# Kernel tuning notes

Hardware: AMD Instinct MI355X
Metric: run time of the kernel (lower is better)

The kernel has to match this reference:

```python
import jax, jax.numpy as jnp
import numpy as np

B, N, IN_C, OUT_C = 32, 1024, 64, 128
ALPHA = 0.2  # LeakyReLU negative slope
NEG_INF = -1e16


def setup_inputs() -> dict:
    key = jax.random.key(0)
    k1, k2, k3, k4, k5 = jax.random.split(key, 5)
    inputs = jax.random.normal(k1, (B, N, IN_C), dtype=jnp.float32)
    # dense 0/1 adjacency mask
    graph = jax.random.randint(k2, (N, N), 0, 2).astype(jnp.float32)
    # torch nn.Linear weight layout: [out_c, in_c]
    W = jax.random.normal(k3, (OUT_C, IN_C), dtype=jnp.float32)
    b = jax.random.normal(k4, (OUT_C,), dtype=jnp.float32)
    a = jax.random.normal(k5, (2 * OUT_C, 1), dtype=jnp.float32)
    return {"inputs": inputs, "graph": graph, "W": W, "b": b, "a": a}


def reference(inputs, graph, W, b, a):
    # h = W(inputs): [B, N, D]
    h = jnp.einsum('bnt,dt->bnd', inputs, W)
    # cat([h_i, h_j]) @ a  ==  h_i @ a1 + h_j @ a2  (decomposed, no [B,N,N,2D] tensor)
    a1 = a[:OUT_C, 0]   # [D]
    a2 = a[OUT_C:, 0]   # [D]
    s1 = jnp.einsum('bnd,d->bn', h, a1)  # score contribution of node i
    s2 = jnp.einsum('bnd,d->bn', h, a2)  # score contribution of node j
    e = s1[:, :, None] + s2[:, None, :]  # [B, N, N]
    e = jnp.where(e > 0, e, ALPHA * e)   # LeakyReLU
    e = e * graph                        # zero out non-edges
    # torch masked_fill_(eq(outputs, 0), -1e16)
    e = jnp.where(e == 0.0, NEG_INF, e)
    attention = jax.nn.softmax(e, axis=2)  # [B, N, N]
    out = jnp.einsum('bij,bjd->bid', attention, h) + b  # [B, N, D]
    return out
```

## Files before the change

kernel.cpp:

```cpp
#include <hip/hip_runtime.h>
#include <hip/hip_bf16.h>

#define ALPHA 0.2f

typedef unsigned short ushort_t;
typedef unsigned int   uint_t;
typedef unsigned short ushort8 __attribute__((ext_vector_type(8)));
typedef uint_t uintv4 __attribute__((ext_vector_type(4)));
typedef float f32x4 __attribute__((ext_vector_type(4)));
typedef __bf16 bf16x8 __attribute__((ext_vector_type(8)));

__device__ __forceinline__ ushort_t f2bf(float f) {
  unsigned u = __float_as_uint(f);
  u += 0x7fffu + ((u >> 16) & 1u);
  return (ushort_t)(u >> 16);
}

__global__ __launch_bounds__(256) void gat_pack_kernel(
    const float* __restrict__ graph, const float* __restrict__ W,
    const float* __restrict__ avec, uint_t* __restrict__ gmask,
    float* __restrict__ u)
{
  const int row = blockIdx.x, t = threadIdx.x;
  __shared__ uint_t nibs[256];
  float4 g = ((const float4*)(graph + (size_t)row * 1024))[t];
  uint_t nib = (g.x != 0.f ? 1u : 0u) | (g.y != 0.f ? 2u : 0u) |
               (g.z != 0.f ? 4u : 0u) | (g.w != 0.f ? 8u : 0u);
  nibs[t] = nib;
  __syncthreads();
  if (t < 32) {
    uint_t wd = 0;
#pragma unroll
    for (int k = 0; k < 8; ++k) wd |= nibs[t * 8 + k] << (4 * k);
    gmask[(size_t)row * 32 + t] = wd;
  }
  if (row == 0 && t < 128) {
    const int k  = t & 63;
    const int ao = (t >> 6) * 128;
    float a0 = 0.f, a1 = 0.f, a2 = 0.f, a3 = 0.f;
    for (int d = 0; d < 128; d += 4) {
      a0 = fmaf(avec[ao + d + 0], W[(d + 0) * 64 + k], a0);
      a1 = fmaf(avec[ao + d + 1], W[(d + 1) * 64 + k], a1);
      a2 = fmaf(avec[ao + d + 2], W[(d + 2) * 64 + k], a2);
      a3 = fmaf(avec[ao + d + 3], W[(d + 3) * 64 + k], a3);
    }
    u[t] = (a0 + a1) + (a2 + a3);
  }
}

__global__ __launch_bounds__(256) void gat_h_kernel(
    const float* __restrict__ inp, const float* __restrict__ W,
    const float* __restrict__ uvec, ushort_t* __restrict__ hT,
    float* __restrict__ s1, float* __restrict__ s2)
{
  const int b  = blockIdx.x >> 5;
  const int n0 = (blockIdx.x & 31) << 5;
  const int t  = threadIdx.x;
  const int d  = t & 127;
  const int nh = t >> 7;

  __shared__ float    x_lds[32][68];
  __shared__ float    u_lds[128];
  __shared__ ushort_t h_tile[128][40];

  float wreg[64];
  {
    const float4* wrow = (const float4*)(W + d * 64);
#pragma unroll
    for (int k = 0; k < 16; ++k) {
      float4 v = wrow[k];
      wreg[4*k+0] = v.x; wreg[4*k+1] = v.y; wreg[4*k+2] = v.z; wreg[4*k+3] = v.w;
    }
  }
  if (t < 128) u_lds[t] = uvec[t];

  {
    const float4* xsrc = (const float4*)(inp + ((size_t)b * 1024 + n0) * 64);
#pragma unroll
    for (int k = 0; k < 2; ++k) {
      const int g = k * 256 + t;
      const int n = g >> 4, c = g & 15;
      *(float4*)&x_lds[n][c * 4] = xsrc[g];
    }
  }
  __syncthreads();

  for (int r = 0; r < 16; ++r) {
    const int n = nh * 16 + r;
    const float* xr = &x_lds[n][0];
    float ax = 0.f, ay = 0.f, az = 0.f, aw = 0.f;
#pragma unroll
    for (int k = 0; k < 16; ++k) {
      float4 xv = *(const float4*)&xr[4 * k];
      ax = fmaf(wreg[4*k+0], xv.x, ax);
      ay = fmaf(wreg[4*k+1], xv.y, ay);
      az = fmaf(wreg[4*k+2], xv.z, az);
      aw = fmaf(wreg[4*k+3], xv.w, aw);
    }
    h_tile[d][n] = f2bf((ax + ay) + (az + aw));
  }

  if (t < 64) {
    const int n = t & 31, which = t >> 5;
    const float* xr = &x_lds[n][0];
    const float* uu = &u_lds[which * 64];
    float a0 = 0.f, a1 = 0.f, a2 = 0.f, a3 = 0.f;
#pragma unroll
    for (int k = 0; k < 16; ++k) {
      float4 xv = *(const float4*)&xr[4 * k];
      a0 = fmaf(xv.x, uu[4*k+0], a0);
      a1 = fmaf(xv.y, uu[4*k+1], a1);
      a2 = fmaf(xv.z, uu[4*k+2], a2);
      a3 = fmaf(xv.w, uu[4*k+3], a3);
    }
    const float sv = (a0 + a1) + (a2 + a3);
    if (which == 0) s1[(size_t)b * 1024 + n0 + n] = sv;
    else            s2[(size_t)b * 1024 + n0 + n] = sv;
  }
  __syncthreads();

#pragma unroll
  for (int it = 0; it < 2; ++it) {
    const int idx = it * 256 + t;
    const int d2  = idx >> 2;
    const int ch  = (idx & 3) * 8;
    ushort8 v = *(const ushort8*)&h_tile[d2][ch];
    *(ushort8*)(hT + ((size_t)b * 128 + d2) * 1024 + n0 + ch) = v;
  }
}

__global__ __launch_bounds__(256) void gat_attn_kernel(
    const uint_t* __restrict__ gmask, const ushort_t* __restrict__ hT,
    const float* __restrict__ s1g, const float* __restrict__ s2g,
    const float* __restrict__ bias, float* __restrict__ out)
{
  const int ic = blockIdx.x;
  const int b  = blockIdx.y;
  const int i0 = ic << 6;
  const int t  = threadIdx.x;
  const int w  = t >> 6;
  const int rg = w & 1;
  const int jh = w >> 1;
  const int l  = t & 63;
  const int rl = l & 15;
  const int js = (l >> 4) * 8;

  __shared__ float  s2_lds[1024];
  __shared__ uint_t mask_lds[64][33];
  __shared__ float  red_part[64][4];
  __shared__ float  red_row[64];
  __shared__ float  credu[64][132];
  __shared__ float  den_lds[64];

  ((float4*)s2_lds)[t] = ((const float4*)(s2g + (size_t)b * 1024))[t];
  {
    const uint4* gsrc = (const uint4*)(gmask + (size_t)i0 * 32);
#pragma unroll
    for (int k2 = 0; k2 < 2; ++k2) {
      const int idx = t + k2 * 256;
      uint4 mv = gsrc[idx];
      const int mr = idx >> 3, mc = (idx & 7) * 4;
      mask_lds[mr][mc + 0] = mv.x; mask_lds[mr][mc + 1] = mv.y;
      mask_lds[mr][mc + 2] = mv.z; mask_lds[mr][mc + 3] = mv.w;
    }
  }
  __syncthreads();

  {
    const int irow = t >> 2, bo = (t & 3) * 8;
    float mx = -1e30f;
    for (int jt = 0; jt < 32; ++jt) {
      const uint_t wd = mask_lds[irow][jt] >> bo;
      const float4 sA = *(const float4*)(s2_lds + jt * 32 + bo);
      const float4 sB = *(const float4*)(s2_lds + jt * 32 + bo + 4);
      if (wd & 1u)   mx = fmaxf(mx, sA.x);
      if (wd & 2u)   mx = fmaxf(mx, sA.y);
      if (wd & 4u)   mx = fmaxf(mx, sA.z);
      if (wd & 8u)   mx = fmaxf(mx, sA.w);
      if (wd & 16u)  mx = fmaxf(mx, sB.x);
      if (wd & 32u)  mx = fmaxf(mx, sB.y);
      if (wd & 64u)  mx = fmaxf(mx, sB.z);
      if (wd & 128u) mx = fmaxf(mx, sB.w);
    }
    red_part[irow][t & 3] = mx;
  }
  __syncthreads();
  if (t < 64)
    red_row[t] = fmaxf(fmaxf(red_part[t][0], red_part[t][1]),
                       fmaxf(red_part[t][2], red_part[t][3]));
  __syncthreads();

  const int ib = rg * 32;
  const float s1lo = s1g[(size_t)b * 1024 + i0 + ib + rl];
  const float s1hi = s1g[(size_t)b * 1024 + i0 + ib + 16 + rl];
  const float tl = s1lo + red_row[ib + rl];
  const float th = s1hi + red_row[ib + 16 + rl];
  const float Milo = tl > 0.f ? tl : ALPHA * tl;
  const float Mihi = th > 0.f ? th : ALPHA * th;

  const ushort_t* hb =
      hT + (size_t)b * 128 * 1024 + (size_t)rl * 1024 + jh * 512 + js;

  f32x4 c[2][8];
#pragma unroll
  for (int is = 0; is < 2; ++is)
#pragma unroll
    for (int ds = 0; ds < 8; ++ds) c[is][ds] = f32x4{0.f, 0.f, 0.f, 0.f};
  float den_lo = 0.f, den_hi = 0.f;

  ushort8 bv[8], nb[8];
#pragma unroll
  for (int ds = 0; ds < 8; ++ds)
    bv[ds] = *(const ushort8*)(hb + (size_t)ds * 16 * 1024);

  for (int jt = 0; jt < 16; ++jt) {
    const int j0 = jt * 32;
    const int jn = (jt + 1 < 16) ? j0 + 32 : j0;
#pragma unroll
    for (int ds = 0; ds < 8; ++ds)
      nb[ds] = *(const ushort8*)(hb + (size_t)ds * 16 * 1024 + jn);

    const uint_t wlo = mask_lds[ib + rl][jh * 16 + jt] >> js;
    const uint_t whi = mask_lds[ib + 16 + rl][jh * 16 + jt] >> js;
    const float4 sA = *(const float4*)(s2_lds + jh * 512 + j0 + js);
    const float4 sB = *(const float4*)(s2_lds + jh * 512 + j0 + js + 4);
    const float sv[8] = {sA.x, sA.y, sA.z, sA.w, sB.x, sB.y, sB.z, sB.w};
    float plo[8], phi[8];
#pragma unroll
    for (int e = 0; e < 8; ++e) {
      float te = s1lo + sv[e];
      float v  = fmaxf(te, ALPHA * te);
      plo[e] = (((wlo >> e) & 1u) && v != 0.f) ? __expf(v - Milo) : 0.f;
      te = s1hi + sv[e];
      v  = fmaxf(te, ALPHA * te);
      phi[e] = (((whi >> e) & 1u) && v != 0.f) ? __expf(v - Mihi) : 0.f;
    }
    uint_t pkl[4], pkh[4];
#pragma unroll
    for (int q = 0; q < 4; ++q) {
      asm("v_cvt_pk_bf16_f32 %0, %1, %2"
          : "=v"(pkl[q]) : "v"(plo[2 * q]), "v"(plo[2 * q + 1]));
      asm("v_cvt_pk_bf16_f32 %0, %1, %2"
          : "=v"(pkh[q]) : "v"(phi[2 * q]), "v"(phi[2 * q + 1]));
      den_lo += __uint_as_float(pkl[q] << 16) +
                __uint_as_float(pkl[q] & 0xffff0000u);
      den_hi += __uint_as_float(pkh[q] << 16) +
                __uint_as_float(pkh[q] & 0xffff0000u);
    }
    const bf16x8 av0 =
        __builtin_bit_cast(bf16x8, (uintv4){pkl[0], pkl[1], pkl[2], pkl[3]});
    const bf16x8 av1 =
        __builtin_bit_cast(bf16x8, (uintv4){pkh[0], pkh[1], pkh[2], pkh[3]});
    __builtin_amdgcn_s_setprio(1);
#pragma unroll
    for (int ds = 0; ds < 8; ++ds) {
      const bf16x8 bvv = __builtin_bit_cast(bf16x8, bv[ds]);
      c[0][ds] = __builtin_amdgcn_mfma_f32_16x16x32_bf16(av0, bvv, c[0][ds], 0, 0, 0);
      c[1][ds] = __builtin_amdgcn_mfma_f32_16x16x32_bf16(av1, bvv, c[1][ds], 0, 0, 0);
    }
    __builtin_amdgcn_s_setprio(0);
#pragma unroll
    for (int ds = 0; ds < 8; ++ds) bv[ds] = nb[ds];
  }

  den_lo += __shfl_xor(den_lo, 16); den_lo += __shfl_xor(den_lo, 32);
  den_hi += __shfl_xor(den_hi, 16); den_hi += __shfl_xor(den_hi, 32);

  if (jh == 1) {
#pragma unroll
    for (int is = 0; is < 2; ++is)
#pragma unroll
      for (int ds = 0; ds < 8; ++ds)
#pragma unroll
        for (int r = 0; r < 4; ++r)
          credu[ib + is * 16 + (l >> 4) * 4 + r][ds * 16 + rl] = c[is][ds][r];
    if (l < 16) {
      den_lds[ib + rl]      = den_lo;
      den_lds[ib + 16 + rl] = den_hi;
    }
  }
  __syncthreads();
  if (jh == 0) {
    const float dl = den_lo + den_lds[ib + rl];
    const float dh = den_hi + den_lds[ib + 16 + rl];
    const float inv_lo = dl > 0.f ? 1.f / dl : 0.f;
    const float inv_hi = dh > 0.f ? 1.f / dh : 0.f;
#pragma unroll
    for (int ds = 0; ds < 8; ++ds) {
      const int col = ds * 16 + rl;
      const float bc = bias[col];
#pragma unroll
      for (int is = 0; is < 2; ++is) {
#pragma unroll
        for (int r = 0; r < 4; ++r) {
          const int rr  = (l >> 4) * 4 + r;
          const int row = ib + is * 16 + rr;
          const float cc = c[is][ds][r] + credu[row][col];
          const float iv = __shfl(is ? inv_hi : inv_lo, rr);
          out[((size_t)b * 1024 + i0 + row) * 128 + col] = fmaf(cc, iv, bc);
        }
      }
    }
  }
}

extern "C" void kernel_launch(void* const* d_in, const int* in_sizes, int n_in,
                              void* d_out, int out_size, void* d_ws, size_t ws_size,
                              hipStream_t stream) {
  (void)in_sizes; (void)n_in; (void)out_size; (void)ws_size;
  const float* inp   = (const float*)d_in[0];
  const float* graph = (const float*)d_in[1];
  const float* W     = (const float*)d_in[2];
  const float* bias  = (const float*)d_in[3];
  const float* avec  = (const float*)d_in[4];
  float* out = (float*)d_out;

  char* ws = (char*)d_ws;
  ushort_t* hT = (ushort_t*)ws;
  float* s1    = (float*)(ws + (size_t)8 * 1024 * 1024);
  float* s2    = s1 + 32 * 1024;
  float* u     = s2 + 32 * 1024;
  uint_t* gm   = (uint_t*)(ws + (size_t)8 * 1024 * 1024 + 512 * 1024);

  gat_pack_kernel<<<1024, 256, 0, stream>>>(graph, W, avec, gm, u);
  gat_h_kernel<<<1024, 256, 0, stream>>>(inp, W, u, hT, s1, s2);
  gat_attn_kernel<<<dim3(16, 32), 256, 0, stream>>>(gm, hT, s1, s2, bias, out);
}
```

Baseline: 75.40 us.

## Compute softmax denominator via MFMA with ones, prefetch mask/s2 and split max chains

The softmax denominator is now accumulated by two extra MFMAs against a vector of bf16 ones, replacing the scalar bf16 unpack-and-add and the cross-lane shuffles. The per-tile mask words and s2 values are loaded from LDS one iteration ahead, overlapping LDS latency with compute. The row-max loop keeps four independent accumulators to break the serial fmax dependency chain. This adds 2 MFMAs per tile (about 12% more matrix work) and extra registers for the prefetched values, in exchange for fewer VALU ops and shorter dependency chains.

Result: no change. 74.51 us (-1.2%).

```diff
diff --git a/kernel.cpp b/kernel.cpp
--- a/kernel.cpp
+++ b/kernel.cpp
@@ -168,21 +168,27 @@
 
   {
     const int irow = t >> 2, bo = (t & 3) * 8;
-    float mx = -1e30f;
-    for (int jt = 0; jt < 32; ++jt) {
-      const uint_t wd = mask_lds[irow][jt] >> bo;
-      const float4 sA = *(const float4*)(s2_lds + jt * 32 + bo);
-      const float4 sB = *(const float4*)(s2_lds + jt * 32 + bo + 4);
-      if (wd & 1u)   mx = fmaxf(mx, sA.x);
-      if (wd & 2u)   mx = fmaxf(mx, sA.y);
-      if (wd & 4u)   mx = fmaxf(mx, sA.z);
-      if (wd & 8u)   mx = fmaxf(mx, sA.w);
-      if (wd & 16u)  mx = fmaxf(mx, sB.x);
-      if (wd & 32u)  mx = fmaxf(mx, sB.y);
-      if (wd & 64u)  mx = fmaxf(mx, sB.z);
-      if (wd & 128u) mx = fmaxf(mx, sB.w);
-    }
-    red_part[irow][t & 3] = mx;
+    float mxa[4] = {-1e30f, -1e30f, -1e30f, -1e30f};
+    for (int jt4 = 0; jt4 < 8; ++jt4) {
+#pragma unroll
+      for (int q = 0; q < 4; ++q) {
+        const int jt = jt4 * 4 + q;
+        const uint_t wd = mask_lds[irow][jt] >> bo;
+        const float4 sA = *(const float4*)(s2_lds + jt * 32 + bo);
+        const float4 sB = *(const float4*)(s2_lds + jt * 32 + bo + 4);
+        float m = mxa[q];
+        if (wd & 1u)   m = fmaxf(m, sA.x);
+        if (wd & 2u)   m = fmaxf(m, sA.y);
+        if (wd & 4u)   m = fmaxf(m, sA.z);
+        if (wd & 8u)   m = fmaxf(m, sA.w);
+        if (wd & 16u)  m = fmaxf(m, sB.x);
+        if (wd & 32u)  m = fmaxf(m, sB.y);
+        if (wd & 64u)  m = fmaxf(m, sB.z);
+        if (wd & 128u) m = fmaxf(m, sB.w);
+        mxa[q] = m;
+      }
+    }
+    red_part[irow][t & 3] = fmaxf(fmaxf(mxa[0], mxa[1]), fmaxf(mxa[2], mxa[3]));
   }
   __syncthreads();
   if (t < 64)
@@ -206,12 +212,19 @@
   for (int is = 0; is < 2; ++is)
 #pragma unroll
     for (int ds = 0; ds < 8; ++ds) c[is][ds] = f32x4{0.f, 0.f, 0.f, 0.f};
-  float den_lo = 0.f, den_hi = 0.f;
+  f32x4 cden[2] = {f32x4{0.f, 0.f, 0.f, 0.f}, f32x4{0.f, 0.f, 0.f, 0.f}};
+  const bf16x8 bones = __builtin_bit_cast(
+      bf16x8, (uintv4){0x3F803F80u, 0x3F803F80u, 0x3F803F80u, 0x3F803F80u});
 
   ushort8 bv[8], nb[8];
 #pragma unroll
   for (int ds = 0; ds < 8; ++ds)
     bv[ds] = *(const ushort8*)(hb + (size_t)ds * 16 * 1024);
+
+  uint_t wlo_c = mask_lds[ib + rl][jh * 16];
+  uint_t whi_c = mask_lds[ib + 16 + rl][jh * 16];
+  float4 sA_c = *(const float4*)(s2_lds + jh * 512 + js);
+  float4 sB_c = *(const float4*)(s2_lds + jh * 512 + js + 4);
 
   for (int jt = 0; jt < 16; ++jt) {
     const int j0 = jt * 32;
@@ -219,12 +232,16 @@
 #pragma unroll
     for (int ds = 0; ds < 8; ++ds)
       nb[ds] = *(const ushort8*)(hb + (size_t)ds * 16 * 1024 + jn);
-
-    const uint_t wlo = mask_lds[ib + rl][jh * 16 + jt] >> js;
-    const uint_t whi = mask_lds[ib + 16 + rl][jh * 16 + jt] >> js;
-    const float4 sA = *(const float4*)(s2_lds + jh * 512 + j0 + js);
-    const float4 sB = *(const float4*)(s2_lds + jh * 512 + j0 + js + 4);
-    const float sv[8] = {sA.x, sA.y, sA.z, sA.w, sB.x, sB.y, sB.z, sB.w};
+    const int jtn = (jt + 1 < 16) ? jt + 1 : jt;
+    const uint_t wlo_n = mask_lds[ib + rl][jh * 16 + jtn];
+    const uint_t whi_n = mask_lds[ib + 16 + rl][jh * 16 + jtn];
+    const float4 sA_n = *(const float4*)(s2_lds + jh * 512 + jtn * 32 + js);
+    const float4 sB_n = *(const float4*)(s2_lds + jh * 512 + jtn * 32 + js + 4);
+
+    const uint_t wlo = wlo_c >> js;
+    const uint_t whi = whi_c >> js;
+    const float sv[8] = {sA_c.x, sA_c.y, sA_c.z, sA_c.w,
+                         sB_c.x, sB_c.y, sB_c.z, sB_c.w};
     float plo[8], phi[8];
 #pragma unroll
     for (int e = 0; e < 8; ++e) {
@@ -242,10 +259,6 @@
           : "=v"(pkl[q]) : "v"(plo[2 * q]), "v"(plo[2 * q + 1]));
       asm("v_cvt_pk_bf16_f32 %0, %1, %2"
           : "=v"(pkh[q]) : "v"(phi[2 * q]), "v"(phi[2 * q + 1]));
-      den_lo += __uint_as_float(pkl[q] << 16) +
-                __uint_as_float(pkl[q] & 0xffff0000u);
-      den_hi += __uint_as_float(pkh[q] << 16) +
-                __uint_as_float(pkh[q] & 0xffff0000u);
     }
     const bf16x8 av0 =
         __builtin_bit_cast(bf16x8, (uintv4){pkl[0], pkl[1], pkl[2], pkl[3]});
@@ -258,13 +271,13 @@
       c[0][ds] = __builtin_amdgcn_mfma_f32_16x16x32_bf16(av0, bvv, c[0][ds], 0, 0, 0);
       c[1][ds] = __builtin_amdgcn_mfma_f32_16x16x32_bf16(av1, bvv, c[1][ds], 0, 0, 0);
     }
+    cden[0] = __builtin_amdgcn_mfma_f32_16x16x32_bf16(av0, bones, cden[0], 0, 0, 0);
+    cden[1] = __builtin_amdgcn_mfma_f32_16x16x32_bf16(av1, bones, cden[1], 0, 0, 0);
     __builtin_amdgcn_s_setprio(0);
 #pragma unroll
     for (int ds = 0; ds < 8; ++ds) bv[ds] = nb[ds];
-  }
-
-  den_lo += __shfl_xor(den_lo, 16); den_lo += __shfl_xor(den_lo, 32);
-  den_hi += __shfl_xor(den_hi, 16); den_hi += __shfl_xor(den_hi, 32);
+    wlo_c = wlo_n; whi_c = whi_n; sA_c = sA_n; sB_c = sB_n;
+  }
 
   if (jh == 1) {
 #pragma unroll
@@ -274,17 +287,24 @@
 #pragma unroll
         for (int r = 0; r < 4; ++r)
           credu[ib + is * 16 + (l >> 4) * 4 + r][ds * 16 + rl] = c[is][ds][r];
-    if (l < 16) {
-      den_lds[ib + rl]      = den_lo;
-      den_lds[ib + 16 + rl] = den_hi;
+    if (rl == 0) {
+#pragma unroll
+      for (int is = 0; is < 2; ++is)
+#pragma unroll
+        for (int r = 0; r < 4; ++r)
+          den_lds[ib + is * 16 + (l >> 4) * 4 + r] = cden[is][r];
     }
   }
   __syncthreads();
   if (jh == 0) {
-    const float dl = den_lo + den_lds[ib + rl];
-    const float dh = den_hi + den_lds[ib + 16 + rl];
-    const float inv_lo = dl > 0.f ? 1.f / dl : 0.f;
-    const float inv_hi = dh > 0.f ? 1.f / dh : 0.f;
+    float inv[2][4];
+#pragma unroll
+    for (int is = 0; is < 2; ++is)
+#pragma unroll
+      for (int r = 0; r < 4; ++r) {
+        const float dt = cden[is][r] + den_lds[ib + is * 16 + (l >> 4) * 4 + r];
+        inv[is][r] = dt > 0.f ? 1.f / dt : 0.f;
+      }
 #pragma unroll
     for (int ds = 0; ds < 8; ++ds) {
       const int col = ds * 16 + rl;
@@ -293,11 +313,10 @@
       for (int is = 0; is < 2; ++is) {
 #pragma unroll
         for (int r = 0; r < 4; ++r) {
-          const int rr  = (l >> 4) * 4 + r;
-          const int row = ib + is * 16 + rr;
+          const int row = ib + is * 16 + (l >> 4) * 4 + r;
           const float cc = c[is][ds][r] + credu[row][col];
-          const float iv = __shfl(is ? inv_hi : inv_lo, rr);
-          out[((size_t)b * 1024 + i0 + row) * 128 + col] = fmaf(cc, iv, bc);
+          out[((size_t)b * 1024 + i0 + row) * 128 + col] =
+              fmaf(cc, inv[is][r], bc);
         }
       }
     }
```
